# Performance work log

Hardware: AMD Instinct MI355X
Metric: run time of the kernel (lower is better)

Reference implementation:

```python
import jax, jax.numpy as jnp
import numpy as np
from jax import lax

EPS = 1e-5

def conv3x3(x, w, b):
    # x: [N,C,H,W], w: [O,I,3,3]
    y = lax.conv_general_dilated(x, w, window_strides=(1, 1), padding='SAME',
                                 dimension_numbers=('NCHW', 'OIHW', 'NCHW'))
    return y + b[None, :, None, None]

def batchnorm(x, gamma, beta):
    # training-mode BN: batch statistics over (N,H,W), biased variance
    mean = x.mean(axis=(0, 2, 3), keepdims=True)
    var = x.var(axis=(0, 2, 3), keepdims=True)
    xn = (x - mean) * lax.rsqrt(var + EPS)
    return xn * gamma[None, :, None, None] + beta[None, :, None, None]

def instance_norm_unbiased(x):
    # per-(sample, channel) mean and unbiased std (torch .std() default ddof=1)
    n = x.shape[2] * x.shape[3]
    m = x.mean(axis=(2, 3), keepdims=True)
    var = ((x - m) ** 2).sum(axis=(2, 3), keepdims=True) / (n - 1)
    return (x - m) / jnp.sqrt(var)

def res_block(x, w, b, g, be):
    # w: [2,64,64,3,3]; b,g,be: [2,64]
    h = x
    for k in range(2):
        h = jax.nn.celu(batchnorm(conv3x3(h, w[k], b[k]), g[k], be[k]))
    return h + x

def setup_inputs() -> dict:
    key = jax.random.key(0)
    ks = jax.random.split(key, 8)
    x = jax.random.normal(ks[0], (8, 3, 256, 256), dtype=jnp.float32)
    w1 = jax.random.normal(ks[1], (64, 6, 3, 3), dtype=jnp.float32) * 0.05
    b1 = jnp.zeros((64,), jnp.float32)
    g1 = jnp.ones((64,), jnp.float32)
    be1 = jnp.zeros((64,), jnp.float32)
    bw = jax.random.normal(ks[2], (3, 2, 64, 64, 3, 3), dtype=jnp.float32) * 0.02
    bb = jnp.zeros((3, 2, 64), jnp.float32)
    bg = jnp.ones((3, 2, 64), jnp.float32)
    bbe = jnp.zeros((3, 2, 64), jnp.float32)
    w2 = jax.random.normal(ks[3], (3, 64, 3, 3), dtype=jnp.float32) * 0.05
    b2 = jnp.zeros((3,), jnp.float32)
    return {"x": x, "w1": w1, "b1": b1, "g1": g1, "be1": be1,
            "bw": bw, "bb": bb, "bg": bg, "bbe": bbe, "w2": w2, "b2": b2}

def reference(x, w1, b1, g1, be1, bw, bb, bg, bbe, w2, b2):
    normalized = instance_norm_unbiased(x)
    inp = jnp.concatenate([x, normalized], axis=1)  # [N,6,H,W]
    out = jax.nn.celu(batchnorm(conv3x3(inp, w1, b1), g1, be1))
    for i in range(3):  # 3 structurally distinct ResBlocks
        out = res_block(out, bw[i], bb[i], bg[i], bbe[i])
    out = jax.nn.celu(conv3x3(out, w2, b2))
    return out + x
```

## Files before the change

kernel.cpp:

```cpp
#include <hip/hip_runtime.h>
#include <cstdint>
#include <cstddef>

#define DEVI __device__ __forceinline__

static constexpr int HW = 65536;
static constexpr float PTOTF = 524288.0f;
static constexpr int NPB = 8192;

typedef __attribute__((ext_vector_type(8))) short bfx8;
typedef __attribute__((ext_vector_type(16))) float fx16;
typedef __attribute__((ext_vector_type(4))) float fx4;

DEVI unsigned short f2bf(float f) {
  unsigned int x = __float_as_uint(f);
  x += 0x7fffu + ((x >> 16) & 1u);
  return (unsigned short)(x >> 16);
}
DEVI float celuf(float v) { return v > 0.0f ? v : expm1f(v); }

DEVI void unpack8(const uint4 u, float* v) {
  v[0] = __uint_as_float(u.x << 16); v[1] = __uint_as_float(u.x & 0xffff0000u);
  v[2] = __uint_as_float(u.y << 16); v[3] = __uint_as_float(u.y & 0xffff0000u);
  v[4] = __uint_as_float(u.z << 16); v[5] = __uint_as_float(u.z & 0xffff0000u);
  v[6] = __uint_as_float(u.w << 16); v[7] = __uint_as_float(u.w & 0xffff0000u);
}

DEVI void gload16(const unsigned short* g, unsigned short* l) {
  __builtin_amdgcn_global_load_lds(
      (const __attribute__((address_space(1))) unsigned int*)g,
      (__attribute__((address_space(3))) unsigned int*)l, 16, 0, 0);
}

DEVI size_t padpx(int n, int h, int w) {
  return ((size_t)n * 258 + (h + 1)) * 258 + (w + 1);
}

__global__ __launch_bounds__(256)
void k_prep(const float* __restrict__ w1, const float* __restrict__ bw,
            const float* __restrict__ w2, float* __restrict__ wt1,
            unsigned short* __restrict__ wtm, unsigned short* __restrict__ wlast,
            unsigned short* a, unsigned short* b, unsigned short* c) {
  int id = blockIdx.x * 256 + threadIdx.x;
  if (id < 24672) {
    const int buf = id / 8224, r = id - buf * 8224;
    const int n = r / 1028, k = r - n * 1028;
    int hp, wp;
    if (k < 258)      { hp = 0;           wp = k; }
    else if (k < 516) { hp = 257;         wp = k - 258; }
    else if (k < 772) { hp = k - 516 + 1; wp = 0; }
    else              { hp = k - 772 + 1; wp = 257; }
    unsigned short* p = (buf == 0 ? a : buf == 1 ? b : c) +
                        (((size_t)n * 258 + hp) * 258 + wp) * 64;
    const uint4 z = {0, 0, 0, 0};
#pragma unroll
    for (int q = 0; q < 8; ++q) ((uint4*)p)[q] = z;
    return;
  }
  id -= 24672;
  if (id < 221184) {
    const int cv = id / 36864, r = id - cv * 36864;
    const int tap = r >> 12, rr = r & 4095, oc = rr >> 6, ic = rr & 63;
    const float v = bw[((size_t)cv * 4096 + oc * 64 + ic) * 9 + tap];
    const int dic = ((((ic >> 3) ^ (oc & 7)) << 3) | (ic & 7));
    wtm[(size_t)cv * 36864 + tap * 4096 + oc * 64 + dic] = f2bf(v);
    return;
  }
  id -= 221184;
  if (id < 4608) {
    const int tap = id / 512, rr = id - tap * 512, ic = rr >> 6, oc = rr & 63;
    wt1[id] = (ic < 6) ? w1[(oc * 6 + ic) * 9 + tap] : 0.0f;
    return;
  }
  id -= 4608;
  if (id < 9216) {
    const int cch = id >> 9, r = id & 511, l = r >> 3, j = r & 7;
    const int oc = l & 15, kg = l >> 4;
    const int tap = cch >> 1, kc = cch & 1;
    const int ic = kc * 32 + kg * 8 + j;
    wlast[id] = (oc < 3) ? f2bf(w2[(oc * 64 + ic) * 9 + tap]) : (unsigned short)0;
  }
}

__global__ __launch_bounds__(256)
void k_inorm(const float* __restrict__ x, float* __restrict__ ms) {
  __shared__ float s1[256], s2[256];
  const int b = blockIdx.x;
  const float4* p = (const float4*)(x + (size_t)b * HW);
  float sum = 0.f, sq = 0.f;
  for (int j = threadIdx.x; j < HW / 4; j += 256) {
    const float4 v = p[j];
    sum += v.x + v.y + v.z + v.w;
    sq  += v.x * v.x + v.y * v.y + v.z * v.z + v.w * v.w;
  }
  s1[threadIdx.x] = sum; s2[threadIdx.x] = sq;
  __syncthreads();
  for (int s = 128; s > 0; s >>= 1) {
    if ((int)threadIdx.x < s) {
      s1[threadIdx.x] += s1[threadIdx.x + s];
      s2[threadIdx.x] += s2[threadIdx.x + s];
    }
    __syncthreads();
  }
  if (threadIdx.x == 0) {
    const float m = s1[0] * (1.0f / HW);
    const float var = (s2[0] - s1[0] * s1[0] * (1.0f / HW)) * (1.0f / (HW - 1));
    ms[2 * b] = m;
    ms[2 * b + 1] = rsqrtf(var);
  }
}

__global__ __launch_bounds__(256)
void k_conv1(const float* __restrict__ x, const float* __restrict__ ms,
             const float* __restrict__ wt, unsigned short* __restrict__ out,
             float* __restrict__ psum, float* __restrict__ psq) {
  __shared__ float in_s[3 * 66 * 9];
  __shared__ float w_s[9 * 8 * 64];
  __shared__ float red0[16][64], red1[16][64];

  const int t = threadIdx.x;
  const int b = blockIdx.x;
  const int n = b >> 10;
  const int h = (b >> 2) & 255;
  const int w0 = (b & 3) << 6;

  const float m0 = ms[6 * n + 0], r0 = ms[6 * n + 1];
  const float m1 = ms[6 * n + 2], r1 = ms[6 * n + 3];
  const float m2 = ms[6 * n + 4], r2 = ms[6 * n + 5];

  const int oc0 = (t & 15) * 4;
  const int px0 = (t >> 4) * 4;
  float acc[4][4] = {{0.f}};

  {
    const float4* wsrc = (const float4*)wt;
    for (int j4 = t; j4 < 1152; j4 += 256) ((float4*)w_s)[j4] = wsrc[j4];
  }
  if (t < 198) {
    const int dh = t / 66, px = t - dh * 66;
    const int gh = h + dh - 1, gw = w0 + px - 1;
    const bool ok = ((unsigned)gh < 256u) && ((unsigned)gw < 256u);
    float v[8];
    if (ok) {
      const float* xp = x + (size_t)n * 3 * HW + gh * 256 + gw;
      const float a0 = xp[0], a1 = xp[HW], a2 = xp[2 * HW];
      v[0] = a0; v[1] = a1; v[2] = a2;
      v[3] = (a0 - m0) * r0; v[4] = (a1 - m1) * r1; v[5] = (a2 - m2) * r2;
      v[6] = 0.f; v[7] = 0.f;
    } else {
#pragma unroll
      for (int q = 0; q < 8; ++q) v[q] = 0.f;
    }
    float* d = &in_s[(dh * 66 + px) * 9];
#pragma unroll
    for (int q = 0; q < 8; ++q) d[q] = v[q];
  }
  __syncthreads();
#pragma unroll
  for (int i = 0; i < 8; ++i) {
    float xv[3][6];
#pragma unroll
    for (int dh = 0; dh < 3; ++dh)
#pragma unroll
      for (int j = 0; j < 6; ++j)
        xv[dh][j] = in_s[(dh * 66 + px0 + j) * 9 + i];
#pragma unroll
    for (int dh = 0; dh < 3; ++dh)
#pragma unroll
      for (int dw = 0; dw < 3; ++dw) {
        const float4 wv = *(const float4*)&w_s[((dh * 3 + dw) * 8 + i) * 64 + oc0];
#pragma unroll
        for (int p = 0; p < 4; ++p) {
          const float xin = xv[dh][p + dw];
          acc[p][0] += xin * wv.x;
          acc[p][1] += xin * wv.y;
          acc[p][2] += xin * wv.z;
          acc[p][3] += xin * wv.w;
        }
      }
  }
  unsigned short* ob = out + (((size_t)n * 258 + (h + 1)) * 258 + (w0 + 1)) * 64;
#pragma unroll
  for (int p = 0; p < 4; ++p) {
    ushort4 o;
    o.x = f2bf(acc[p][0]); o.y = f2bf(acc[p][1]);
    o.z = f2bf(acc[p][2]); o.w = f2bf(acc[p][3]);
    *(ushort4*)(ob + (size_t)(px0 + p) * 64 + oc0) = o;
  }
#pragma unroll
  for (int q = 0; q < 4; ++q) {
    float s = 0.f, qv = 0.f;
#pragma unroll
    for (int p = 0; p < 4; ++p) { s += acc[p][q]; qv += acc[p][q] * acc[p][q]; }
    red0[t >> 4][oc0 + q] = s;
    red1[t >> 4][oc0 + q] = qv;
  }
  __syncthreads();
  if (t < 64) {
    float s = 0.f, qv = 0.f;
#pragma unroll
    for (int g2 = 0; g2 < 16; ++g2) { s += red0[g2][t]; qv += red1[g2][t]; }
    psum[(size_t)t * NPB + b] = s;
    psq[(size_t)t * NPB + b]  = qv;
  }
}

__global__ __launch_bounds__(512)
void k_mconv(const unsigned short* __restrict__ in,
             const unsigned short* __restrict__ wt,
             unsigned short* __restrict__ out,
             float* __restrict__ psum, float* __restrict__ psq) {
  __shared__ __align__(16) unsigned short w_s[36864];
  __shared__ __align__(16) unsigned short a_s[2][16896];
  __shared__ float s_red[2][2][2][64];

  const int t = threadIdx.x;
  const int lane = t & 63, wv = t >> 6;
  const int l31 = lane & 31, hi = lane >> 5;
  const int row = wv >> 2;
  const int m   = (wv >> 1) & 1;
  const int p   = wv & 1;
  const int bo = blockIdx.x;
  const int b = (bo & 7) * 64 + (bo >> 3);
  const int n  = b >> 6;
  const int hb = (b >> 2) & 15;
  const int w0 = (b & 3) * 64;
  const int oc0 = m * 32;

#pragma unroll
  for (int j = 0; j < 9; ++j) {
    const int id = t + j * 512;
    gload16(wt + (size_t)id * 8, w_s + (size_t)id * 8);
  }
  auto stage = [&](int buf, int k) {
    const size_t ibase = ((size_t)n * 258 + (hb * 16 + k * 2)) * 258 + w0;
#pragma unroll
    for (int j = 0; j < 5; ++j) {
      const int id = t + j * 512;
      if (id < 2112) {
        const int r = id / 528, c = id - r * 528;
        const int px = c >> 3;
        const int R = r * 66 + px;
        const int sl = (c & 7) ^ (R & 7);
        gload16(in + (ibase + (size_t)r * 258 + px) * 64 + sl * 8,
                &a_s[buf][(size_t)id * 8]);
      }
    }
  };
  stage(0, 0);
  __syncthreads();

  float sv[16] = {0.f}, qv[16] = {0.f};
  const int pxl = p * 32 + l31;

  for (int k = 0; k < 8; ++k) {
    const int cur = k & 1;
    if (k < 7) stage(cur ^ 1, k + 1);
    __builtin_amdgcn_sched_barrier(0);

    fx16 acc = {};
#pragma unroll
    for (int tap = 0; tap < 9; ++tap) {
      const int dh = tap / 3, dw = tap - dh * 3;
      const int R = (row + dh) * 66 + pxl + dw;
      const int oc = oc0 + l31;
#pragma unroll
      for (int ks = 0; ks < 4; ++ks) {
        const int slA = (ks * 2 + hi) ^ (R & 7);
        const bfx8 bf = *(const bfx8*)((const char*)a_s[cur] +
                                       (size_t)R * 128 + (slA << 4));
        const int slW = (ks * 2 + hi) ^ (oc & 7);
        const bfx8 wf = *(const bfx8*)((const char*)w_s +
                                       ((size_t)tap * 4096 + oc * 64) * 2 + (slW << 4));
        acc = __builtin_amdgcn_mfma_f32_32x32x16_bf16(wf, bf, acc, 0, 0, 0);
      }
    }

    const size_t obase = (((size_t)n * 258 + (hb * 16 + k * 2 + row + 1)) * 258 +
                          (w0 + 1)) * 64;
#pragma unroll
    for (int q = 0; q < 4; ++q) {
      const int ocb = oc0 + q * 8 + 4 * hi;
      ushort4 o;
      o.x = f2bf(acc[q * 4 + 0]);
      o.y = f2bf(acc[q * 4 + 1]);
      o.z = f2bf(acc[q * 4 + 2]);
      o.w = f2bf(acc[q * 4 + 3]);
      *(ushort4*)(out + obase + (size_t)pxl * 64 + ocb) = o;
    }
#pragma unroll
    for (int r2 = 0; r2 < 16; ++r2) {
      sv[r2] += acc[r2];
      qv[r2] += acc[r2] * acc[r2];
    }

    asm volatile("s_waitcnt vmcnt(4)" ::: "memory");
    __builtin_amdgcn_sched_barrier(0);
    __builtin_amdgcn_s_barrier();
    __builtin_amdgcn_sched_barrier(0);
  }

#pragma unroll
  for (int st = 1; st <= 16; st <<= 1)
#pragma unroll
    for (int r2 = 0; r2 < 16; ++r2) {
      sv[r2] += __shfl_xor(sv[r2], st);
      qv[r2] += __shfl_xor(qv[r2], st);
    }
  if (l31 == 0) {
#pragma unroll
    for (int r2 = 0; r2 < 16; ++r2) {
      const int oc = oc0 + (r2 & 3) + 8 * (r2 >> 2) + 4 * hi;
      s_red[0][row][p][oc] = sv[r2];
      s_red[1][row][p][oc] = qv[r2];
    }
  }
  __syncthreads();
  if (t < 64) {
    const float s = s_red[0][0][0][t] + s_red[0][0][1][t] +
                    s_red[0][1][0][t] + s_red[0][1][1][t];
    const float q2 = s_red[1][0][0][t] + s_red[1][0][1][t] +
                     s_red[1][1][0][t] + s_red[1][1][1][t];
    psum[(size_t)t * NPB + bo] = s;
    psq [(size_t)t * NPB + bo] = q2;
  }
}

__global__ __launch_bounds__(256)
void k_bnfin(const float* __restrict__ psum, const float* __restrict__ psq,
             const float* __restrict__ g, const float* __restrict__ be,
             float* __restrict__ bnp, int nb) {
  __shared__ float s1[256], s2[256];
  const int c = blockIdx.x;
  const int t = threadIdx.x;
  float s = 0.f, q = 0.f;
  for (int j = t; j < nb; j += 256) {
    s += psum[(size_t)c * NPB + j];
    q += psq[(size_t)c * NPB + j];
  }
  s1[t] = s; s2[t] = q;
  __syncthreads();
  for (int st = 128; st > 0; st >>= 1) {
    if (t < st) { s1[t] += s1[t + st]; s2[t] += s2[t + st]; }
    __syncthreads();
  }
  if (t == 0) {
    const float m = s1[0] / PTOTF;
    const float var = s2[0] / PTOTF - m * m;
    const float sc = g[c] * rsqrtf(var + 1e-5f);
    bnp[c] = sc;
    bnp[64 + c] = be[c] - m * sc;
  }
}

template<int RES>
__global__ __launch_bounds__(256)
void k_apply(const unsigned short* __restrict__ y, const float* __restrict__ bnp,
             unsigned short* __restrict__ a) {
  const size_t gid = (size_t)blockIdx.x * 256 + threadIdx.x;
  const int px = (int)(gid >> 3);
  const int c0 = ((int)gid & 7) * 8;
  const int n = px >> 16, hh = (px >> 8) & 255, ww = px & 255;
  const size_t i = padpx(n, hh, ww) * 64 + c0;
  float v[8];
  unpack8(*(const uint4*)(y + i), v);
  const float4 sa = *(const float4*)(bnp + c0);
  const float4 sb = *(const float4*)(bnp + c0 + 4);
  const float4 ha = *(const float4*)(bnp + 64 + c0);
  const float4 hb = *(const float4*)(bnp + 64 + c0 + 4);
  const float sc[8] = {sa.x, sa.y, sa.z, sa.w, sb.x, sb.y, sb.z, sb.w};
  const float sh[8] = {ha.x, ha.y, ha.z, ha.w, hb.x, hb.y, hb.z, hb.w};
  float r[8];
#pragma unroll
  for (int q = 0; q < 8; ++q) r[q] = celuf(v[q] * sc[q] + sh[q]);
  if (RES) {
    float av[8];
    unpack8(*(const uint4*)(a + i), av);
#pragma unroll
    for (int q = 0; q < 8; ++q) r[q] += av[q];
  }
  uint4 o;
  o.x = (unsigned)f2bf(r[0]) | ((unsigned)f2bf(r[1]) << 16);
  o.y = (unsigned)f2bf(r[2]) | ((unsigned)f2bf(r[3]) << 16);
  o.z = (unsigned)f2bf(r[4]) | ((unsigned)f2bf(r[5]) << 16);
  o.w = (unsigned)f2bf(r[6]) | ((unsigned)f2bf(r[7]) << 16);
  *(uint4*)(a + i) = o;
}

__global__ __launch_bounds__(256, 2)
void k_last(const unsigned short* __restrict__ a, const float* __restrict__ x,
            const unsigned short* __restrict__ wl, const float* __restrict__ b2,
            float* __restrict__ outp) {
  __shared__ __align__(16) unsigned short a_s[3168 * 8];

  const int t = threadIdx.x;
  const int lane = t & 63, wv = t >> 6;
  int b = blockIdx.x;
  b = (b & 7) * 256 + (b >> 3);
  const int n  = b >> 8;
  const int h0 = ((b >> 2) & 63) * 4;
  const int w0 = (b & 3) * 64;

  const size_t ibase = ((size_t)n * 258 + h0) * 258 + w0;
  for (int seg = wv; seg < 54; seg += 4) {
    const int r = seg / 9;
    const int p = seg - r * 9;
    const int c = p * 64 + lane;
    const int px = c >> 3;
    const int R = r * 66 + px;
    const int sl = (c & 7) ^ (R & 7);
    if (c < 528)
      gload16(a + (ibase + (size_t)r * 258 + px) * 64 + sl * 8,
              a_s + (size_t)(r * 528 + p * 64) * 8);
  }
  __syncthreads();

  const int col = lane & 15, kg = lane >> 4;
  const float bz0 = b2[0], bz1 = b2[1], bz2 = b2[2];
#pragma unroll
  for (int ti = 0; ti < 4; ++ti) {
    fx4 acc = {};
#pragma unroll
    for (int tap = 0; tap < 9; ++tap) {
      const int dh = tap / 3, dw = tap - dh * 3;
      const int px = ti * 16 + col + dw;
      const int R = (wv + dh) * 66 + px;
#pragma unroll
      for (int kc = 0; kc < 2; ++kc) {
        const int s = kc * 4 + kg;
        const bfx8 bf = *(const bfx8*)((const char*)a_s +
            (size_t)R * 128 + ((s ^ (R & 7)) << 4));
        const bfx8 af = *(const bfx8*)(wl + ((size_t)(tap * 2 + kc) * 64 + lane) * 8);
        acc = __builtin_amdgcn_mfma_f32_16x16x32_bf16(af, bf, acc, 0, 0, 0);
      }
    }
    if (kg == 0) {
      const int h = h0 + wv;
      const size_t ob = (size_t)n * 3 * HW + ((size_t)h << 8) + w0 + ti * 16 + col;
      outp[ob]          = celuf(acc[0] + bz0) + x[ob];
      outp[ob + HW]     = celuf(acc[1] + bz1) + x[ob + HW];
      outp[ob + 2 * HW] = celuf(acc[2] + bz2) + x[ob + 2 * HW];
    }
  }
}

extern "C" void kernel_launch(void* const* d_in, const int* in_sizes, int n_in,
                              void* d_out, int out_size, void* d_ws, size_t ws_size,
                              hipStream_t stream) {
  const float* x   = (const float*)d_in[0];
  const float* w1  = (const float*)d_in[1];
  const float* g1  = (const float*)d_in[3];
  const float* be1 = (const float*)d_in[4];
  const float* bw  = (const float*)d_in[5];
  const float* bg  = (const float*)d_in[7];
  const float* bbe = (const float*)d_in[8];
  const float* w2  = (const float*)d_in[9];
  const float* b2  = (const float*)d_in[10];
  float* out = (float*)d_out;

  const size_t PADBUF = (size_t)8 * 258 * 258 * 64 * 2;
  size_t off = 0;
  auto alloc = [&](size_t bytes) {
    size_t cur = off;
    off += (bytes + 255) & ~(size_t)255;
    return cur;
  };
  const size_t oA   = alloc(PADBUF);
  const size_t oB   = alloc(PADBUF);
  const size_t oC   = alloc(PADBUF);
  const size_t oW1  = alloc(4608 * 4);
  const size_t oWM  = alloc((size_t)6 * 36864 * 2);
  const size_t oWL  = alloc(9216 * 2);
  const size_t oMS  = alloc(48 * 4);
  const size_t oBNP = alloc(7 * 128 * 4);
  const size_t oPS  = alloc((size_t)64 * NPB * 4);
  const size_t oPQ  = alloc((size_t)64 * NPB * 4);
  if (off > ws_size) return;

  char* wsb = (char*)d_ws;
  unsigned short* bufA = (unsigned short*)(wsb + oA);
  unsigned short* bufB = (unsigned short*)(wsb + oB);
  unsigned short* bufC = (unsigned short*)(wsb + oC);
  float* wt1 = (float*)(wsb + oW1);
  unsigned short* wtm = (unsigned short*)(wsb + oWM);
  unsigned short* wlast = (unsigned short*)(wsb + oWL);
  float* ms  = (float*)(wsb + oMS);
  float* bnp = (float*)(wsb + oBNP);
  float* psum = (float*)(wsb + oPS);
  float* psq  = (float*)(wsb + oPQ);

  k_prep<<<1015, 256, 0, stream>>>(w1, bw, w2, wt1, wtm, wlast, bufA, bufB, bufC);
  k_inorm<<<24, 256, 0, stream>>>(x, ms);

  k_conv1<<<8192, 256, 0, stream>>>(x, ms, wt1, bufB, psum, psq);
  k_bnfin<<<64, 256, 0, stream>>>(psum, psq, g1, be1, bnp, 8192);
  k_apply<0><<<16384, 256, 0, stream>>>(bufB, bnp, bufA);

  for (int i = 0; i < 3; ++i) {
    const int s1 = 1 + 2 * i, s2 = 2 + 2 * i;
    k_mconv<<<512, 512, 0, stream>>>(bufA, wtm + (size_t)(2 * i) * 36864,
                                     bufB, psum, psq);
    k_bnfin<<<64, 256, 0, stream>>>(psum, psq, bg + (size_t)(2 * i) * 64,
        bbe + (size_t)(2 * i) * 64, bnp + (size_t)s1 * 128, 512);
    k_apply<0><<<16384, 256, 0, stream>>>(bufB, bnp + (size_t)s1 * 128, bufC);
    k_mconv<<<512, 512, 0, stream>>>(bufC, wtm + (size_t)(2 * i + 1) * 36864,
                                     bufB, psum, psq);
    k_bnfin<<<64, 256, 0, stream>>>(psum, psq, bg + (size_t)(2 * i + 1) * 64,
        bbe + (size_t)(2 * i + 1) * 64, bnp + (size_t)s2 * 128, 512);
    k_apply<1><<<16384, 256, 0, stream>>>(bufB, bnp + (size_t)s2 * 128, bufA);
  }

  k_last<<<2048, 256, 0, stream>>>(bufA, x, wlast, b2, out);
}
```

Before: 744.8 us.

## Restructure mid conv with row ring buffer and 2x2 MFMA tiles, split BN stats

The 3x3 64->64 conv kernel changes from 512 threads with per-wave 1x1 MFMA tiles over 8 two-row steps to 256 threads where each wave computes a 2x2 block of 32x32 MFMA tiles. Input rows stream through a 10-row LDS ring buffer instead of a double buffer, so halo rows are reused across steps and fragment reuse per load improves. BN statistics are moved out of the conv epilogue into a separate k_bnstats kernel that rereads the bf16 output. This lightens the conv's register and epilogue load, at the cost of an extra kernel launch and a full reread of the activation per conv.

```diff
diff --git a/kernel.cpp b/kernel.cpp
--- a/kernel.cpp
+++ b/kernel.cpp
@@ -205,124 +205,146 @@
   }
 }
 
-__global__ __launch_bounds__(512)
+__global__ __launch_bounds__(256)
 void k_mconv(const unsigned short* __restrict__ in,
              const unsigned short* __restrict__ wt,
-             unsigned short* __restrict__ out,
-             float* __restrict__ psum, float* __restrict__ psq) {
+             unsigned short* __restrict__ out) {
   __shared__ __align__(16) unsigned short w_s[36864];
-  __shared__ __align__(16) unsigned short a_s[2][16896];
-  __shared__ float s_red[2][2][2][64];
+  __shared__ __align__(16) unsigned short ring[10 * 528 * 8];
 
   const int t = threadIdx.x;
   const int lane = t & 63, wv = t >> 6;
   const int l31 = lane & 31, hi = lane >> 5;
-  const int row = wv >> 2;
-  const int m   = (wv >> 1) & 1;
-  const int p   = wv & 1;
   const int bo = blockIdx.x;
   const int b = (bo & 7) * 64 + (bo >> 3);
   const int n  = b >> 6;
   const int hb = (b >> 2) & 15;
   const int w0 = (b & 3) * 64;
-  const int oc0 = m * 32;
-
-#pragma unroll
-  for (int j = 0; j < 9; ++j) {
-    const int id = t + j * 512;
+
+#pragma unroll
+  for (int j = 0; j < 18; ++j) {
+    const int id = t + j * 256;
     gload16(wt + (size_t)id * 8, w_s + (size_t)id * 8);
   }
-  auto stage = [&](int buf, int k) {
-    const size_t ibase = ((size_t)n * 258 + (hb * 16 + k * 2)) * 258 + w0;
-#pragma unroll
-    for (int j = 0; j < 5; ++j) {
-      const int id = t + j * 512;
-      if (id < 2112) {
+  {
+    const size_t gb = ((size_t)n * 258 + hb * 16) * 258 + w0;
+#pragma unroll
+    for (int j = 0; j < 13; ++j) {
+      const int id = t + j * 256;
+      if (id < 3168) {
         const int r = id / 528, c = id - r * 528;
         const int px = c >> 3;
         const int R = r * 66 + px;
         const int sl = (c & 7) ^ (R & 7);
-        gload16(in + (ibase + (size_t)r * 258 + px) * 64 + sl * 8,
-                &a_s[buf][(size_t)id * 8]);
+        gload16(in + (gb + (size_t)r * 258 + px) * 64 + sl * 8,
+                ring + (size_t)id * 8);
       }
     }
-  };
-  stage(0, 0);
-  __syncthreads();
-
-  float sv[16] = {0.f}, qv[16] = {0.f};
-  const int pxl = p * 32 + l31;
-
-  for (int k = 0; k < 8; ++k) {
-    const int cur = k & 1;
-    if (k < 7) stage(cur ^ 1, k + 1);
-    __builtin_amdgcn_sched_barrier(0);
-
-    fx16 acc = {};
-#pragma unroll
-    for (int tap = 0; tap < 9; ++tap) {
-      const int dh = tap / 3, dw = tap - dh * 3;
-      const int R = (row + dh) * 66 + pxl + dw;
-      const int oc = oc0 + l31;
-#pragma unroll
-      for (int ks = 0; ks < 4; ++ks) {
-        const int slA = (ks * 2 + hi) ^ (R & 7);
-        const bfx8 bf = *(const bfx8*)((const char*)a_s[cur] +
-                                       (size_t)R * 128 + (slA << 4));
-        const int slW = (ks * 2 + hi) ^ (oc & 7);
-        const bfx8 wf = *(const bfx8*)((const char*)w_s +
-                                       ((size_t)tap * 4096 + oc * 64) * 2 + (slW << 4));
-        acc = __builtin_amdgcn_mfma_f32_32x32x16_bf16(wf, bf, acc, 0, 0, 0);
-      }
-    }
-
-    const size_t obase = (((size_t)n * 258 + (hb * 16 + k * 2 + row + 1)) * 258 +
-                          (w0 + 1)) * 64;
-#pragma unroll
-    for (int q = 0; q < 4; ++q) {
-      const int ocb = oc0 + q * 8 + 4 * hi;
-      ushort4 o;
-      o.x = f2bf(acc[q * 4 + 0]);
-      o.y = f2bf(acc[q * 4 + 1]);
-      o.z = f2bf(acc[q * 4 + 2]);
-      o.w = f2bf(acc[q * 4 + 3]);
-      *(ushort4*)(out + obase + (size_t)pxl * 64 + ocb) = o;
-    }
-#pragma unroll
-    for (int r2 = 0; r2 < 16; ++r2) {
-      sv[r2] += acc[r2];
-      qv[r2] += acc[r2] * acc[r2];
-    }
-
-    asm volatile("s_waitcnt vmcnt(4)" ::: "memory");
+  }
+
+  for (int k = 0; k < 4; ++k) {
+    if (k == 0) { asm volatile("s_waitcnt vmcnt(0)" ::: "memory"); }
+    else       { asm volatile("s_waitcnt vmcnt(16)" ::: "memory"); }
     __builtin_amdgcn_sched_barrier(0);
     __builtin_amdgcn_s_barrier();
     __builtin_amdgcn_sched_barrier(0);
-  }
-
-#pragma unroll
-  for (int st = 1; st <= 16; st <<= 1)
-#pragma unroll
-    for (int r2 = 0; r2 < 16; ++r2) {
-      sv[r2] += __shfl_xor(sv[r2], st);
-      qv[r2] += __shfl_xor(qv[r2], st);
-    }
-  if (l31 == 0) {
-#pragma unroll
-    for (int r2 = 0; r2 < 16; ++r2) {
-      const int oc = oc0 + (r2 & 3) + 8 * (r2 >> 2) + 4 * hi;
-      s_red[0][row][p][oc] = sv[r2];
-      s_red[1][row][p][oc] = qv[r2];
-    }
-  }
+    if (k < 3) {
+      const int base = 4 * k + 6;
+#pragma unroll
+      for (int j = 0; j < 9; ++j) {
+        const int id = t + j * 256;
+        if (id < 2112) {
+          const int r = id / 528, c = id - r * 528;
+          const int Lr = base + r;
+          const int s = (Lr >= 10) ? Lr - 10 : Lr;
+          const int px = c >> 3;
+          const int R = s * 66 + px;
+          const int sl = (c & 7) ^ (R & 7);
+          gload16(in + (((size_t)n * 258 + hb * 16 + Lr) * 258 + w0 + px) * 64 + sl * 8,
+                  ring + ((size_t)s * 528 + c) * 8);
+        }
+      }
+    }
+    __builtin_amdgcn_sched_barrier(0);
+
+    fx16 acc[2][2] = {};
+#pragma unroll
+    for (int tap = 0; tap < 9; ++tap) {
+      const int dh = tap / 3, dw = tap - dh * 3;
+      const int Lr = 4 * k + wv + dh;
+      const int s = (Lr >= 10) ? Lr - 10 : Lr;
+      const int Rbase = s * 66 + dw;
+#pragma unroll
+      for (int ks = 0; ks < 4; ++ks) {
+        bfx8 wf[2], bf[2];
+#pragma unroll
+        for (int m = 0; m < 2; ++m) {
+          const int oc = m * 32 + l31;
+          const int slW = (ks * 2 + hi) ^ (oc & 7);
+          wf[m] = *(const bfx8*)((const char*)w_s +
+                   ((size_t)tap * 4096 + oc * 64) * 2 + (slW << 4));
+        }
+#pragma unroll
+        for (int p = 0; p < 2; ++p) {
+          const int R = Rbase + p * 32 + l31;
+          const int slA = (ks * 2 + hi) ^ (R & 7);
+          bf[p] = *(const bfx8*)((const char*)ring + (size_t)R * 128 + (slA << 4));
+        }
+#pragma unroll
+        for (int m = 0; m < 2; ++m)
+#pragma unroll
+          for (int p = 0; p < 2; ++p)
+            acc[m][p] = __builtin_amdgcn_mfma_f32_32x32x16_bf16(
+                wf[m], bf[p], acc[m][p], 0, 0, 0);
+      }
+    }
+
+    const int orow = hb * 16 + 4 * k + wv + 1;
+    const size_t obase = (((size_t)n * 258 + orow) * 258 + (w0 + 1)) * 64;
+#pragma unroll
+    for (int m = 0; m < 2; ++m)
+#pragma unroll
+      for (int p = 0; p < 2; ++p) {
+        const int px = p * 32 + l31;
+#pragma unroll
+        for (int q = 0; q < 4; ++q) {
+          const int ocb = m * 32 + q * 8 + 4 * hi;
+          ushort4 o;
+          o.x = f2bf(acc[m][p][q * 4 + 0]);
+          o.y = f2bf(acc[m][p][q * 4 + 1]);
+          o.z = f2bf(acc[m][p][q * 4 + 2]);
+          o.w = f2bf(acc[m][p][q * 4 + 3]);
+          *(ushort4*)(out + obase + (size_t)px * 64 + ocb) = o;
+        }
+      }
+  }
+}
+
+__global__ __launch_bounds__(256)
+void k_bnstats(const unsigned short* __restrict__ y, float* __restrict__ psum,
+               float* __restrict__ psq) {
+  __shared__ float r0[32][64], r1[32][64];
+  const int b = blockIdx.x, t = threadIdx.x;
+  const int c8 = (t & 7) * 8, pg = t >> 3;
+  float sv[8] = {0.f}, qv[8] = {0.f};
+#pragma unroll
+  for (int j = 0; j < 16; ++j) {
+    const int px = b * 512 + pg * 16 + j;
+    const int n = px >> 16, hh = (px >> 8) & 255, ww = px & 255;
+    float v[8];
+    unpack8(*(const uint4*)(y + padpx(n, hh, ww) * 64 + c8), v);
+#pragma unroll
+    for (int q = 0; q < 8; ++q) { sv[q] += v[q]; qv[q] += v[q] * v[q]; }
+  }
+#pragma unroll
+  for (int q = 0; q < 8; ++q) { r0[pg][c8 + q] = sv[q]; r1[pg][c8 + q] = qv[q]; }
   __syncthreads();
   if (t < 64) {
-    const float s = s_red[0][0][0][t] + s_red[0][0][1][t] +
-                    s_red[0][1][0][t] + s_red[0][1][1][t];
-    const float q2 = s_red[1][0][0][t] + s_red[1][0][1][t] +
-                     s_red[1][1][0][t] + s_red[1][1][1][t];
-    psum[(size_t)t * NPB + bo] = s;
-    psq [(size_t)t * NPB + bo] = q2;
+    float s = 0.f, q2 = 0.f;
+#pragma unroll
+    for (int g = 0; g < 32; ++g) { s += r0[g][t]; q2 += r1[g][t]; }
+    psum[(size_t)t * NPB + b] = s;
+    psq [(size_t)t * NPB + b] = q2;
   }
 }
 
@@ -498,15 +520,15 @@
 
   for (int i = 0; i < 3; ++i) {
     const int s1 = 1 + 2 * i, s2 = 2 + 2 * i;
-    k_mconv<<<512, 512, 0, stream>>>(bufA, wtm + (size_t)(2 * i) * 36864,
-                                     bufB, psum, psq);
+    k_mconv<<<512, 256, 0, stream>>>(bufA, wtm + (size_t)(2 * i) * 36864, bufB);
+    k_bnstats<<<1024, 256, 0, stream>>>(bufB, psum, psq);
     k_bnfin<<<64, 256, 0, stream>>>(psum, psq, bg + (size_t)(2 * i) * 64,
-        bbe + (size_t)(2 * i) * 64, bnp + (size_t)s1 * 128, 512);
+        bbe + (size_t)(2 * i) * 64, bnp + (size_t)s1 * 128, 1024);
     k_apply<0><<<16384, 256, 0, stream>>>(bufB, bnp + (size_t)s1 * 128, bufC);
-    k_mconv<<<512, 512, 0, stream>>>(bufC, wtm + (size_t)(2 * i + 1) * 36864,
-                                     bufB, psum, psq);
+    k_mconv<<<512, 256, 0, stream>>>(bufC, wtm + (size_t)(2 * i + 1) * 36864, bufB);
+    k_bnstats<<<1024, 256, 0, stream>>>(bufB, psum, psq);
     k_bnfin<<<64, 256, 0, stream>>>(psum, psq, bg + (size_t)(2 * i + 1) * 64,
-        bbe + (size_t)(2 * i + 1) * 64, bnp + (size_t)s2 * 128, 512);
+        bbe + (size_t)(2 * i + 1) * 64, bnp + (size_t)s2 * 128, 1024);
     k_apply<1><<<16384, 256, 0, stream>>>(bufB, bnp + (size_t)s2 * 128, bufA);
   }
 
```

Measured after the change: 750.9 us. About the same (+0.8%).
